# Kernel tuning notes

Measured on AMD Instinct MI355X. Metric: run time of the kernel, lower is better.

## Reference

```python
import jax, jax.numpy as jnp
import numpy as np

# dims
B, L, S, V, C = 128, 50, 100, 100000, 1000   # batch, max_nodes_len, max_session_len, n_items, n_categories
D, DC, H, ND = 64, 64, 64, 4                 # embedding_dim_i, embedding_dim_c, hidden_size, n_demand


def setup_inputs() -> dict:
    key = jax.random.key(0)
    ks = jax.random.split(key, 16)
    inp = {}
    inp['nodes'] = jax.random.randint(ks[0], (B, L), 0, V, dtype=jnp.int32)
    inp['categories'] = jax.random.randint(ks[1], (B, S), 0, C, dtype=jnp.int32)
    inp['adj'] = jax.random.uniform(ks[2], (B, L, L), dtype=jnp.float32)
    inp['nodes_categories'] = jax.random.uniform(ks[3], (B, L, S), dtype=jnp.float32)
    inp['session_last_item_index'] = jax.random.randint(ks[4], (B,), 0, L, dtype=jnp.int32)
    inp['candidate_category'] = jax.random.randint(ks[5], (V,), 0, C, dtype=jnp.int32)
    inp['mask_node'] = jnp.ones((B, L), dtype=jnp.int32)
    # learned parameters
    inp['emb_i'] = (0.02 * jax.random.normal(ks[6], (V, D), dtype=jnp.float32)).at[0].set(0.0)  # padding_idx=0
    inp['emb_c'] = 0.02 * jax.random.normal(ks[7], (C, DC), dtype=jnp.float32)
    inp['Wd1'] = 0.05 * jax.random.normal(ks[8], (DC, H), dtype=jnp.float32)
    inp['bd1'] = jnp.zeros((H,), dtype=jnp.float32)
    inp['Wd2'] = 0.05 * jax.random.normal(ks[9], (H, ND), dtype=jnp.float32)
    inp['bd2'] = jnp.zeros((ND,), dtype=jnp.float32)
    inp['W_pvsd'] = 0.05 * jax.random.normal(ks[10], (2 * D, D), dtype=jnp.float32)
    inp['b_pvsd'] = jnp.zeros((D,), dtype=jnp.float32)
    inp['W_im'] = 0.05 * jax.random.normal(ks[11], (D, D), dtype=jnp.float32)
    return inp


def _demand_scores(categories, candidate_category, emb_c, Wd1, bd1, Wd2, bd2):
    # per-session-item demand distribution: (B, ND, S)
    cat_emb = emb_c[categories]                                   # (B,S,DC)
    ds = jax.nn.softmax(jnp.tanh(cat_emb @ Wd1 + bd1) @ Wd2 + bd2, axis=-1)
    demand_score = jnp.swapaxes(ds, 1, 2)                         # (B,ND,S)
    # per-candidate demand distribution: (1, ND, V)
    cand_c = emb_c[candidate_category]                            # (V,DC)
    dsc = jax.nn.softmax(jnp.tanh(cand_c @ Wd1 + bd1) @ Wd2 + bd2, axis=-1)
    demand_score_candidate = dsc.T[None]                          # (1,ND,V)
    return demand_score, demand_score_candidate


def reference(nodes, categories, adj, nodes_categories, session_last_item_index,
              candidate_category, mask_node, emb_i, emb_c, Wd1, bd1, Wd2, bd2,
              W_pvsd, b_pvsd, W_im):
    session_emb = emb_i[nodes]                                    # (B,L,D) gather
    demand_score, demand_score_candidate = _demand_scores(
        categories, candidate_category, emb_c, Wd1, bd1, Wd2, bd2)
    # gnn_mask=True: node representation is the broadcast-expanded session emb
    gnn = jnp.broadcast_to(session_emb[:, None], (B, ND, L, D))   # (B,ND,L,D)
    # graph aggregation: masked mean over nodes
    mask = mask_node.astype(session_emb.dtype)                    # (B,L)
    graph_rep = jnp.einsum('bl,bnld->bnd', mask, gnn) / mask.sum(-1)[:, None, None]  # (B,ND,D)
    # graph infomax (DGI-style bilinear discriminator; negatives = rolled batch)
    pos = jnp.einsum('bnld,de,bne->bnl', gnn, W_im, graph_rep)
    neg = jnp.einsum('bnld,de,bne->bnl', gnn, W_im, jnp.roll(graph_rep, 1, axis=0))
    infomax_loss = -(jax.nn.log_sigmoid(pos).mean() + jax.nn.log_sigmoid(-neg).mean())
    # masked gather of the last-clicked node per session
    idx = session_last_item_index.astype(jnp.int32)[:, None, None, None]
    last = jnp.take_along_axis(gnn, jnp.broadcast_to(idx, (B, ND, 1, D)), axis=2)[:, :, 0, :]  # (B,ND,D)
    session_rep = jnp.concatenate([graph_rep, last], axis=-1)     # (B,ND,2D)
    # PVSD: project session rep, score against all candidate embeddings (no repeat!)
    h = jnp.tanh(session_rep @ W_pvsd + b_pvsd)                   # (B,ND,D)
    P_v_s_d = jnp.einsum('bnd,vd->bnv', h, emb_i)                 # (B,ND,V)
    P_v = jnp.sum(P_v_s_d * demand_score_candidate, axis=1)       # (B,V)
    return (P_v, infomax_loss, gnn)
```

## Files before the change

kernel.cpp:

```cpp
#include <hip/hip_runtime.h>
#include <math.h>

#define B   128
#define L   50
#define V   100000
#define ND  4
#define D   64


typedef __attribute__((ext_vector_type(8))) short s8v;
typedef __attribute__((ext_vector_type(4))) float f4v;

#define NVB ((V + 127) / 128)

__device__ __forceinline__ float log_sigmoid(float x) {
    if (x >= 0.f) return -log1pf(expf(-x));
    return x - log1pf(expf(x));
}

__device__ __forceinline__ short bf16rne(float x) {
    unsigned u = __float_as_uint(x);
    unsigned r = u + 0x7FFFu + ((u >> 16) & 1u);
    return (short)(r >> 16);
}
__device__ __forceinline__ float bf16f(short s) {
    return __uint_as_float(((unsigned)(unsigned short)s) << 16);
}

__global__ __launch_bounds__(256) void k1_fused(
    const int* __restrict__ nodes, const int* __restrict__ mask,
    const int* __restrict__ sli, const float* __restrict__ emb_i,
    const float* __restrict__ W_pvsd, const float* __restrict__ b_pvsd,
    const float* __restrict__ W_im,
    float* __restrict__ gnn_out, float* __restrict__ u,
    short* __restrict__ hh, short* __restrict__ hl,
    float* __restrict__ loss)
{
    const int b = blockIdx.x;
    const int t = threadIdx.x;
    if (b == 0 && t == 0) loss[0] = 0.f;
    __shared__ int   s_nodes[L];
    __shared__ float s_mask[L];
    __shared__ float s_part[4][D];
    __shared__ float s_gr[D], s_last[D];
    if (t < L) {
        s_nodes[t] = nodes[b * L + t];
        s_mask[t]  = (float)mask[b * L + t];
    }
    __syncthreads();
    const int d  = t & 63;
    const int l0 = t >> 6;
    float acc = 0.f;
    for (int l = l0; l < L; l += 4) {
        float val = emb_i[(size_t)s_nodes[l] * D + d];
        size_t o = ((size_t)(b * ND + 0) * L + l) * D + d;
        gnn_out[o]                   = val;
        gnn_out[o + (size_t)L * D]   = val;
        gnn_out[o + 2*(size_t)L * D] = val;
        gnn_out[o + 3*(size_t)L * D] = val;
        acc += s_mask[l] * val;
    }
    s_part[l0][d] = acc;
    __syncthreads();
    if (t < D) {
        float msum = 0.f;
        for (int l = 0; l < L; ++l) msum += s_mask[l];
        float s = s_part[0][t] + s_part[1][t] + s_part[2][t] + s_part[3][t];
        s_gr[t]   = s / msum;
        s_last[t] = emb_i[(size_t)s_nodes[sli[b]] * D + t];
    }
    __syncthreads();
    if (t < D) {
        float uu = 0.f;
        #pragma unroll
        for (int e = 0; e < D; ++e) uu += W_im[t * D + e] * s_gr[e];
        u[b * D + t] = uu;
        float pre = b_pvsd[t];
        #pragma unroll
        for (int k = 0; k < D; ++k) pre += s_gr[k]   * W_pvsd[k * D + t];
        #pragma unroll
        for (int k = 0; k < D; ++k) pre += s_last[k] * W_pvsd[(D + k) * D + t];
        float hv = tanhf(pre);
        short hi = bf16rne(hv);
        short lo = bf16rne(hv - bf16f(hi));
        hh[b * D + t] = hi;
        hl[b * D + t] = lo;
    }
}

__global__ __launch_bounds__(256, 4) void k5_mfma(
    const short* __restrict__ hh, const short* __restrict__ hl,
    const float* __restrict__ emb_i, const float* __restrict__ u,
    const float* __restrict__ gnn, float* __restrict__ pv,
    float* __restrict__ loss)
{
    __shared__ short slds[B * 128];

    const int t = threadIdx.x;

    if (blockIdx.x >= NVB) {
        const int b = blockIdx.x - NVB;
        float* s_up = reinterpret_cast<float*>(slds);
        float* s_un = s_up + D;
        if (t < D) {
            const int bm1 = (b + B - 1) % B;
            s_up[t] = u[b * D + t];
            s_un[t] = u[bm1 * D + t];
        }
        __syncthreads();
        if (t < 64) {
            float lsp = 0.f, lsn = 0.f;
            if (t < L) {
                const float* se = gnn + ((size_t)(b * ND) * L + t) * D;
                float sp = 0.f, sn = 0.f;
                #pragma unroll
                for (int d2 = 0; d2 < D; ++d2) {
                    float vv = se[d2];
                    sp += vv * s_up[d2];
                    sn += vv * s_un[d2];
                }
                lsp = log_sigmoid(sp);
                lsn = log_sigmoid(-sn);
            }
            float tot = lsp + lsn;
            for (int off = 32; off > 0; off >>= 1) tot += __shfl_down(tot, off);
            if (t == 0) atomicAdd(loss, -tot / (float)(B * L));
        }
        return;
    }

    #pragma unroll
    for (int k = 0; k < 8; ++k) {
        const int i   = k * 256 + t;
        const int row = i >> 4;
        const int q   = i & 15;
        const int p   = (q & 8) | ((q & 7) ^ (row & 7));
        const short* src = (q < 8 ? hh : hl) + row * D + (q & 7) * 8;
        *(s8v*)(&slds[row * 128 + p * 8]) = *(const s8v*)(src);
    }
    __syncthreads();

    const int lane = t & 63;
    const int wid  = t >> 6;
    const int lm   = lane & 15;
    const int lg   = lane >> 4;
    const int v0   = (blockIdx.x * 8 + wid * 2) * 16;
    const int vcA  = v0 + lm;
    const int vcB  = v0 + 16 + lm;
    const int vldA = vcA < V ? vcA : (V - 1);
    const int vldB = vcB < V ? vcB : (V - 1);

    const float* epA = emb_i + (size_t)vldA * D + 8 * lg;
    const float* epB = emb_i + (size_t)vldB * D + 8 * lg;
    f4v ea0 = *(const f4v*)(epA),      ea1 = *(const f4v*)(epA + 4);
    f4v ea2 = *(const f4v*)(epA + 32), ea3 = *(const f4v*)(epA + 36);
    f4v eb0 = *(const f4v*)(epB),      eb1 = *(const f4v*)(epB + 4);
    f4v eb2 = *(const f4v*)(epB + 32), eb3 = *(const f4v*)(epB + 36);

    s8v Ahi0, Alo0, Ahi1, Alo1;
    s8v Bhi0, Blo0, Bhi1, Blo1;
    #pragma unroll
    for (int i = 0; i < 4; ++i) {
        { float x = ea0[i]; short h = bf16rne(x); Ahi0[i]   = h; Alo0[i]   = bf16rne(x - bf16f(h)); }
        { float x = ea1[i]; short h = bf16rne(x); Ahi0[i+4] = h; Alo0[i+4] = bf16rne(x - bf16f(h)); }
        { float x = ea2[i]; short h = bf16rne(x); Ahi1[i]   = h; Alo1[i]   = bf16rne(x - bf16f(h)); }
        { float x = ea3[i]; short h = bf16rne(x); Ahi1[i+4] = h; Alo1[i+4] = bf16rne(x - bf16f(h)); }
        { float x = eb0[i]; short h = bf16rne(x); Bhi0[i]   = h; Blo0[i]   = bf16rne(x - bf16f(h)); }
        { float x = eb1[i]; short h = bf16rne(x); Bhi0[i+4] = h; Blo0[i+4] = bf16rne(x - bf16f(h)); }
        { float x = eb2[i]; short h = bf16rne(x); Bhi1[i]   = h; Blo1[i]   = bf16rne(x - bf16f(h)); }
        { float x = eb3[i]; short h = bf16rne(x); Bhi1[i+4] = h; Blo1[i+4] = bf16rne(x - bf16f(h)); }
    }

    #pragma unroll
    for (int bt = 0; bt < 8; ++bt) {
        const int row = 16 * bt + lm;
        const int s   = lm & 7;
        const short* base = &slds[row * 128];
        s8v ah0 = *(const s8v*)(base + (((lg    ) ^ s) * 8));
        s8v ah1 = *(const s8v*)(base + (((lg + 4) ^ s) * 8));
        s8v al0 = *(const s8v*)(base + 64 + (((lg    ) ^ s) * 8));
        s8v al1 = *(const s8v*)(base + 64 + (((lg + 4) ^ s) * 8));
        f4v cA0 = {0.f,0.f,0.f,0.f}, cA1 = {0.f,0.f,0.f,0.f};
        f4v cB0 = {0.f,0.f,0.f,0.f}, cB1 = {0.f,0.f,0.f,0.f};
        cA0 = __builtin_amdgcn_mfma_f32_16x16x32_bf16(ah0, Ahi0, cA0, 0, 0, 0);
        cA1 = __builtin_amdgcn_mfma_f32_16x16x32_bf16(ah1, Ahi1, cA1, 0, 0, 0);
        cB0 = __builtin_amdgcn_mfma_f32_16x16x32_bf16(ah0, Bhi0, cB0, 0, 0, 0);
        cB1 = __builtin_amdgcn_mfma_f32_16x16x32_bf16(ah1, Bhi1, cB1, 0, 0, 0);
        cA0 = __builtin_amdgcn_mfma_f32_16x16x32_bf16(ah0, Alo0, cA0, 0, 0, 0);
        cA1 = __builtin_amdgcn_mfma_f32_16x16x32_bf16(ah1, Alo1, cA1, 0, 0, 0);
        cB0 = __builtin_amdgcn_mfma_f32_16x16x32_bf16(ah0, Blo0, cB0, 0, 0, 0);
        cB1 = __builtin_amdgcn_mfma_f32_16x16x32_bf16(ah1, Blo1, cB1, 0, 0, 0);
        cA0 = __builtin_amdgcn_mfma_f32_16x16x32_bf16(al0, Ahi0, cA0, 0, 0, 0);
        cA1 = __builtin_amdgcn_mfma_f32_16x16x32_bf16(al1, Ahi1, cA1, 0, 0, 0);
        cB0 = __builtin_amdgcn_mfma_f32_16x16x32_bf16(al0, Bhi0, cB0, 0, 0, 0);
        cB1 = __builtin_amdgcn_mfma_f32_16x16x32_bf16(al1, Bhi1, cB1, 0, 0, 0);
        const int br = 16 * bt + 4 * lg;
        if (vcA < V) {
            pv[(size_t)(br + 0) * V + vcA] = cA0[0] + cA1[0];
            pv[(size_t)(br + 1) * V + vcA] = cA0[1] + cA1[1];
            pv[(size_t)(br + 2) * V + vcA] = cA0[2] + cA1[2];
            pv[(size_t)(br + 3) * V + vcA] = cA0[3] + cA1[3];
        }
        if (vcB < V) {
            pv[(size_t)(br + 0) * V + vcB] = cB0[0] + cB1[0];
            pv[(size_t)(br + 1) * V + vcB] = cB0[1] + cB1[1];
            pv[(size_t)(br + 2) * V + vcB] = cB0[2] + cB1[2];
            pv[(size_t)(br + 3) * V + vcB] = cB0[3] + cB1[3];
        }
    }
}

extern "C" void kernel_launch(void* const* d_in, const int* in_sizes, int n_in,
                              void* d_out, int out_size, void* d_ws, size_t ws_size,
                              hipStream_t stream)
{
    const int*   nodes  = (const int*)d_in[0];
    const int*   sli    = (const int*)d_in[4];
    const int*   mask   = (const int*)d_in[6];
    const float* emb_i  = (const float*)d_in[7];
    const float* W_pvsd = (const float*)d_in[13];
    const float* b_pvsd = (const float*)d_in[14];
    const float* W_im   = (const float*)d_in[15];

    float* pv   = (float*)d_out;
    float* loss = pv + (size_t)B * V;
    float* gnn  = loss + 1;

    float* ws = (float*)d_ws;
    float* u  = ws;
    short* hh = (short*)(u + B * D);
    short* hl = hh + B * D;

    k1_fused<<<B, 256, 0, stream>>>(nodes, mask, sli, emb_i, W_pvsd, b_pvsd,
                                    W_im, gnn, u, hh, hl, loss);
    k5_mfma<<<NVB + B, 256, 0, stream>>>(hh, hl, emb_i, u, gnn, pv, loss);
}
```

Measured before the change: 31.95 us.

## Move gnn output broadcast from k1 into extra blocks of main MFMA kernel

The first kernel no longer writes the four-way replicated gnn tensor. That write is now done by extra blocks appended to the MFMA scoring kernel, which issue float4 gather-copies from emb_i. The infomax blocks read embeddings directly via node indices instead of the gnn buffer. The aim is to shorten the serial first kernel and overlap the ~6.5MB gnn write with the large P_v computation, at the cost of more blocks competing for bandwidth in the second launch.

```diff
diff --git a/kernel.cpp b/kernel.cpp
--- a/kernel.cpp
+++ b/kernel.cpp
@@ -12,6 +12,8 @@
 typedef __attribute__((ext_vector_type(4))) float f4v;
 
 #define NVB ((V + 127) / 128)
+#define NIB (B)
+#define NGB ((B * ND * L * (D / 4)) / 256)
 
 __device__ __forceinline__ float log_sigmoid(float x) {
     if (x >= 0.f) return -log1pf(expf(-x));
@@ -27,13 +29,12 @@
     return __uint_as_float(((unsigned)(unsigned short)s) << 16);
 }
 
-__global__ __launch_bounds__(256) void k1_fused(
+__global__ __launch_bounds__(256) void k1_compute(
     const int* __restrict__ nodes, const int* __restrict__ mask,
     const int* __restrict__ sli, const float* __restrict__ emb_i,
     const float* __restrict__ W_pvsd, const float* __restrict__ b_pvsd,
     const float* __restrict__ W_im,
-    float* __restrict__ gnn_out, float* __restrict__ u,
-    short* __restrict__ hh, short* __restrict__ hl,
+    float* __restrict__ u, short* __restrict__ hh, short* __restrict__ hl,
     float* __restrict__ loss)
 {
     const int b = blockIdx.x;
@@ -51,15 +52,8 @@
     const int d  = t & 63;
     const int l0 = t >> 6;
     float acc = 0.f;
-    for (int l = l0; l < L; l += 4) {
-        float val = emb_i[(size_t)s_nodes[l] * D + d];
-        size_t o = ((size_t)(b * ND + 0) * L + l) * D + d;
-        gnn_out[o]                   = val;
-        gnn_out[o + (size_t)L * D]   = val;
-        gnn_out[o + 2*(size_t)L * D] = val;
-        gnn_out[o + 3*(size_t)L * D] = val;
-        acc += s_mask[l] * val;
-    }
+    for (int l = l0; l < L; l += 4)
+        acc += s_mask[l] * emb_i[(size_t)s_nodes[l] * D + d];
     s_part[l0][d] = acc;
     __syncthreads();
     if (t < D) {
@@ -91,27 +85,42 @@
 __global__ __launch_bounds__(256, 4) void k5_mfma(
     const short* __restrict__ hh, const short* __restrict__ hl,
     const float* __restrict__ emb_i, const float* __restrict__ u,
-    const float* __restrict__ gnn, float* __restrict__ pv,
-    float* __restrict__ loss)
+    const int* __restrict__ nodes, float* __restrict__ gnn,
+    float* __restrict__ pv, float* __restrict__ loss)
 {
     __shared__ short slds[B * 128];
 
     const int t = threadIdx.x;
+
+    if (blockIdx.x >= NVB + NIB) {
+        const int idx = (blockIdx.x - NVB - NIB) * 256 + t;
+        const int d4   = idx & (D / 4 - 1);
+        const int rest = idx >> 4;
+        const int l    = rest % L;
+        const int bn   = rest / L;
+        const int b    = bn >> 2;
+        const int node = nodes[b * L + l];
+        reinterpret_cast<float4*>(gnn)[idx] =
+            reinterpret_cast<const float4*>(emb_i)[node * (D / 4) + d4];
+        return;
+    }
 
     if (blockIdx.x >= NVB) {
         const int b = blockIdx.x - NVB;
         float* s_up = reinterpret_cast<float*>(slds);
         float* s_un = s_up + D;
+        int*   s_nd = reinterpret_cast<int*>(s_un + D);
         if (t < D) {
             const int bm1 = (b + B - 1) % B;
             s_up[t] = u[b * D + t];
             s_un[t] = u[bm1 * D + t];
         }
+        if (t < L) s_nd[t] = nodes[b * L + t];
         __syncthreads();
         if (t < 64) {
             float lsp = 0.f, lsn = 0.f;
             if (t < L) {
-                const float* se = gnn + ((size_t)(b * ND) * L + t) * D;
+                const float* se = emb_i + (size_t)s_nd[t] * D;
                 float sp = 0.f, sn = 0.f;
                 #pragma unroll
                 for (int d2 = 0; d2 < D; ++d2) {
@@ -231,7 +240,8 @@
     short* hh = (short*)(u + B * D);
     short* hl = hh + B * D;
 
-    k1_fused<<<B, 256, 0, stream>>>(nodes, mask, sli, emb_i, W_pvsd, b_pvsd,
-                                    W_im, gnn, u, hh, hl, loss);
-    k5_mfma<<<NVB + B, 256, 0, stream>>>(hh, hl, emb_i, u, gnn, pv, loss);
-}
+    k1_compute<<<B, 256, 0, stream>>>(nodes, mask, sli, emb_i, W_pvsd, b_pvsd,
+                                      W_im, u, hh, hl, loss);
+    k5_mfma<<<NVB + NIB + NGB, 256, 0, stream>>>(hh, hl, emb_i, u, nodes,
+                                                 gnn, pv, loss);
+}
```

Result: faster. 30.13 us (-5.7%).
